# Kernel tuning notes

Measured on AMD Instinct MI355X. Metric: run time of the kernel, lower is better.

## Reference

```python
import jax, jax.numpy as jnp
import numpy as np

B, S, E, H = 4, 1024, 2048, 16
D = E // H  # head_dim = 128


def setup_inputs() -> dict:
    key = jax.random.key(0)
    k1, k2, k3, k4, k5 = jax.random.split(key, 5)
    scale = 1.0 / np.sqrt(E)
    return {
        "query": jax.random.normal(k1, (B, S, E), dtype=jnp.float32),
        "in_proj_weight": jax.random.normal(k2, (3 * E, E), dtype=jnp.float32) * scale,
        "in_proj_bias": jax.random.normal(k3, (3 * E,), dtype=jnp.float32) * 0.02,
        "out_proj_weight": jax.random.normal(k4, (E, E), dtype=jnp.float32) * scale,
        "out_proj_bias": jax.random.normal(k5, (E,), dtype=jnp.float32) * 0.02,
    }


def reference(query, in_proj_weight, in_proj_bias, out_proj_weight, out_proj_bias):
    b, s, e = query.shape
    d = e // H
    # fused QKV projection: [B,S,3E]
    proj = jnp.einsum("bse,fe->bsf", query, in_proj_weight) + in_proj_bias
    q, k, v = jnp.split(proj, 3, axis=-1)
    # [B,S,E] -> [B,H,S,D]
    def to_heads(t):
        return t.reshape(b, s, H, d).transpose(0, 2, 1, 3)
    q, k, v = to_heads(q), to_heads(k), to_heads(v)
    # scaled dot-product attention (non-causal, no mask, no dropout)
    scores = jnp.einsum("bhqd,bhkd->bhqk", q, k) / jnp.sqrt(jnp.asarray(d, q.dtype))
    attn = jax.nn.softmax(scores, axis=-1)
    ctx = jnp.einsum("bhqk,bhkd->bhqd", attn, v)
    # [B,H,S,D] -> [B,S,E]
    ctx = ctx.transpose(0, 2, 1, 3).reshape(b, s, e)
    out = jnp.einsum("bse,fe->bsf", ctx, out_proj_weight) + out_proj_bias
    return out
```

## Files before the change

kernel.cpp:

```cpp
#include <hip/hip_runtime.h>
#include <hip/hip_fp16.h>

#define F16 _Float16
typedef F16 f16x8 __attribute__((ext_vector_type(8)));
typedef F16 f16x4 __attribute__((ext_vector_type(4)));
typedef float f32x4 __attribute__((ext_vector_type(4)));

__global__ void cvt_f32_f16(const float* __restrict__ src, F16* __restrict__ dst, int n) {
    int idx = blockIdx.x * blockDim.x + threadIdx.x;
    int stride = gridDim.x * blockDim.x;
    for (int i = idx * 4; i < n; i += stride * 4) {
        float4 v = *reinterpret_cast<const float4*>(src + i);
        f16x4 o;
        o[0] = (F16)v.x; o[1] = (F16)v.y; o[2] = (F16)v.z; o[3] = (F16)v.w;
        *reinterpret_cast<f16x4*>(dst + i) = o;
    }
}

__device__ __forceinline__ void gl_lds16(const F16* g, F16* l) {
    __builtin_amdgcn_global_load_lds(
        (const __attribute__((address_space(1))) void*)g,
        (__attribute__((address_space(3))) void*)l, 16, 0, 0);
}

template <int EPI>
__global__ __launch_bounds__(512, 2) void gemm8(
    const F16* __restrict__ A, const F16* __restrict__ Bw, const float* __restrict__ bias,
    F16* __restrict__ q_ws, F16* __restrict__ k_ws, F16* __restrict__ v_ws,
    float* __restrict__ fout, int M, int N, int K)
{
    __shared__ __align__(16) F16 lds[2][4][8192];
    const int tid = threadIdx.x;
    const int w = tid >> 6, l = tid & 63;
    const int lr = l & 15, lg = l >> 4;
    const int wm = w >> 2, wn = w & 3;

    const int nbn = N >> 8;
    const int cpx = (int)gridDim.x >> 3;
    const int work = ((int)blockIdx.x & 7) * cpx + ((int)blockIdx.x >> 3);
    const int nb = work % nbn, mb = work / nbn;
    const long brow = (long)mb * 256, bcol = (long)nb * 256;

    const F16* rb0 = A + brow * K;
    const F16* rb1 = rb0 + 128 * (long)K;
    const F16* rb2 = Bw + bcol * K;
    const F16* rb3 = rb2 + 128 * (long)K;

    const int sr0 = ((tid >> 7) << 4) + (tid & 15);
    const int skk = (((tid >> 6) & 1) << 5) + (((tid >> 4) & 3) << 3);
    const int wb8 = (w << 6) * 8;

#define GISSUE(BUF, R, S, KT, RB) \
    gl_lds16(RB + (long)(sr0 + S * 64) * K + (KT) * 64 + skk, \
             &lds[BUF][R][S * 4096 + wb8])

    const int NK = K >> 6;

    f32x4 acc[8][4];
#pragma unroll
    for (int f = 0; f < 8; ++f)
#pragma unroll
        for (int nf = 0; nf < 4; ++nf) acc[f][nf] = f32x4{0.f, 0.f, 0.f, 0.f};

    GISSUE(0, 0, 0, 0, rb0); GISSUE(0, 0, 1, 0, rb0);
    GISSUE(0, 1, 0, 0, rb1); GISSUE(0, 1, 1, 0, rb1);
    GISSUE(0, 2, 0, 0, rb2); GISSUE(0, 2, 1, 0, rb2);
    GISSUE(0, 3, 0, 0, rb3); GISSUE(0, 3, 1, 0, rb3);
    if (NK > 1) {
        GISSUE(1, 2, 0, 1, rb2); GISSUE(1, 2, 1, 1, rb2);
        GISSUE(1, 3, 0, 1, rb3); GISSUE(1, 3, 1, 1, rb3);
        GISSUE(1, 0, 0, 1, rb0); GISSUE(1, 1, 0, 1, rb1);
        asm volatile("s_waitcnt vmcnt(6)" ::: "memory");
    } else {
        asm volatile("s_waitcnt vmcnt(0)" ::: "memory");
    }
    __builtin_amdgcn_s_barrier();

    for (int kt = 0; kt < NK; ++kt) {
        const int cur = kt & 1, nxt = cur ^ 1;
        const F16* Areg = &lds[cur][wm][0];
        const F16* Breg = &lds[cur][2 + (wn >> 1)][0];
        f16x8 b[4][2];
#pragma unroll
        for (int nf = 0; nf < 4; ++nf)
#pragma unroll
            for (int ks = 0; ks < 2; ++ks)
                b[nf][ks] = *reinterpret_cast<const f16x8*>(
                    Breg + ((((wn & 1) * 4 + nf) * 2 + ks) * 64 + l) * 8);
#pragma unroll
        for (int p = 0; p < 4; ++p) {
            f16x8 a[2][2];
#pragma unroll
            for (int mf = 0; mf < 2; ++mf)
#pragma unroll
                for (int ks = 0; ks < 2; ++ks)
                    a[mf][ks] = *reinterpret_cast<const f16x8*>(
                        Areg + (((2 * p + mf) * 2 + ks) * 64 + l) * 8);
            if (p == 0) {
                if (kt + 1 < NK) { GISSUE(nxt, 0, 1, kt + 1, rb0); GISSUE(nxt, 1, 1, kt + 1, rb1); }
            } else if (p == 1) {
                if (kt + 2 < NK) { GISSUE(cur, 2, 0, kt + 2, rb2); GISSUE(cur, 2, 1, kt + 2, rb2); }
            } else if (p == 2) {
                if (kt + 2 < NK) { GISSUE(cur, 3, 0, kt + 2, rb3); GISSUE(cur, 3, 1, kt + 2, rb3); }
            } else {
                if (kt + 2 < NK) { GISSUE(cur, 0, 0, kt + 2, rb0); GISSUE(cur, 1, 0, kt + 2, rb1); }
            }
            __builtin_amdgcn_sched_barrier(0);
            __builtin_amdgcn_s_barrier();
            asm volatile("s_waitcnt lgkmcnt(0)" ::: "memory");
            __builtin_amdgcn_sched_barrier(0);
            __builtin_amdgcn_s_setprio(1);
#pragma unroll
            for (int mf = 0; mf < 2; ++mf)
#pragma unroll
                for (int nf = 0; nf < 4; ++nf)
#pragma unroll
                    for (int ks = 0; ks < 2; ++ks)
                        acc[2 * p + mf][nf] = __builtin_amdgcn_mfma_f32_16x16x32_f16(
                            a[mf][ks], b[nf][ks], acc[2 * p + mf][nf], 0, 0, 0);
            __builtin_amdgcn_s_setprio(0);
            __builtin_amdgcn_sched_barrier(0);
            if (p == 3) {
                if (kt + 2 < NK) asm volatile("s_waitcnt vmcnt(6)" ::: "memory");
                else             asm volatile("s_waitcnt vmcnt(0)" ::: "memory");
            }
            __builtin_amdgcn_s_barrier();
        }
    }
#undef GISSUE

    const int col0 = (int)bcol + wn * 64;
    const int row0 = (int)brow + wm * 128;
    if constexpr (EPI == 0) {
        const int part = (int)(bcol >> 11);
        const int bI = row0 >> 10;
        const int sb = row0 & 1023;
        const float scl = (part == 0) ? 0.08838834764831845f : 1.0f;
#pragma unroll
        for (int nf = 0; nf < 4; ++nf) {
            const int gcol = col0 + nf * 16 + lr;
            const float bv = bias[gcol];
            const int d = gcol & 127;
            const int hh = (gcol >> 7) & 15;
            if (part == 2) {
                F16* dst0 = v_ws + ((long)((bI * 16 + hh) * 128 + d)) * 1024;
#pragma unroll
                for (int f = 0; f < 8; ++f) {
                    f16x4 pv;
#pragma unroll
                    for (int r = 0; r < 4; ++r) pv[r] = (F16)(acc[f][nf][r] + bv);
                    *reinterpret_cast<f16x4*>(dst0 + sb + f * 16 + lg * 4) = pv;
                }
            } else {
                F16* dst0 = ((part == 0) ? q_ws : k_ws) + ((long)(bI * 16 + hh) * 1024) * 128 + d;
#pragma unroll
                for (int f = 0; f < 8; ++f)
#pragma unroll
                    for (int r = 0; r < 4; ++r)
                        dst0[(long)(sb + f * 16 + lg * 4 + r) * 128] =
                            (F16)((acc[f][nf][r] + bv) * scl);
            }
        }
    } else {
#pragma unroll
        for (int nf = 0; nf < 4; ++nf) {
            const int gcol = col0 + nf * 16 + lr;
            const float bv = bias[gcol];
#pragma unroll
            for (int f = 0; f < 8; ++f)
#pragma unroll
                for (int r = 0; r < 4; ++r)
                    fout[(long)(row0 + f * 16 + lg * 4 + r) * N + gcol] = acc[f][nf][r] + bv;
        }
    }
}

__global__ __launch_bounds__(256, 2) void attn_kernel(
    const F16* __restrict__ q_ws, const F16* __restrict__ k_ws,
    const F16* __restrict__ v_ws, F16* __restrict__ ctx)
{
    __shared__ __align__(16) F16 kt[2][64 * 128];
    __shared__ __align__(16) F16 vt[2][128 * 64];
    __shared__ __align__(16) F16 p_lds[4][2048];
    const int tid = threadIdx.x;
    const int w = tid >> 6, l = tid & 63;
    const int lr = l & 15, lg = l >> 4;
    const int work = (blockIdx.x & 7) * 64 + (blockIdx.x >> 3);
    const int bh = work >> 3, qt = work & 7;
    const int b = bh >> 4, h = bh & 15;
    const int q0 = qt * 128 + w * 32;

    const F16* kbh = k_ws + (long)bh * 1024 * 128;
    const F16* vbh = v_ws + (long)bh * 128 * 1024;

    f16x8 qf[2][4];
#pragma unroll
    for (int mi = 0; mi < 2; ++mi)
#pragma unroll
        for (int ks = 0; ks < 4; ++ks)
            qf[mi][ks] = *reinterpret_cast<const f16x8*>(
                q_ws + ((long)bh * 1024 + q0 + mi * 16 + lr) * 128 + ks * 32 + lg * 8);

    auto stage = [&](int buf, int kv0) {
#pragma unroll
        for (int t = 0; t < 4; ++t) {
            const int chunk = t * 256 + tid;
            const int row = chunk >> 4;
            const int colb = (chunk & 15) << 4;
            const int gcol = colb ^ ((row & 7) << 4);
            gl_lds16(kbh + (long)(kv0 + row) * 128 + (gcol >> 1),
                     &kt[buf][(t * 256 + w * 64) * 8]);
        }
#pragma unroll
        for (int t = 0; t < 4; ++t) {
            const int chunk = t * 256 + tid;
            const int d = chunk >> 3;
            const int colb = (chunk & 7) << 4;
            const int gcol = colb ^ ((d & 7) << 4);
            gl_lds16(vbh + (long)d * 1024 + kv0 + (gcol >> 1),
                     &vt[buf][(t * 256 + w * 64) * 8]);
        }
    };

    float mrun[2][4], lsum[2][4];
#pragma unroll
    for (int mi = 0; mi < 2; ++mi)
#pragma unroll
        for (int r = 0; r < 4; ++r) { mrun[mi][r] = -1e30f; lsum[mi][r] = 0.f; }
    f32x4 acc[2][8];
#pragma unroll
    for (int mi = 0; mi < 2; ++mi)
#pragma unroll
        for (int nf = 0; nf < 8; ++nf) acc[mi][nf] = f32x4{0.f, 0.f, 0.f, 0.f};

    stage(0, 0);
    __syncthreads();
    int cur = 0;
    for (int it = 0; it < 16; ++it) {
        if (it + 1 < 16) stage(cur ^ 1, (it + 1) * 64);

        f32x4 sc[2][4];
#pragma unroll
        for (int mi = 0; mi < 2; ++mi)
#pragma unroll
            for (int cf = 0; cf < 4; ++cf) sc[mi][cf] = f32x4{0.f, 0.f, 0.f, 0.f};
#pragma unroll
        for (int cf = 0; cf < 4; ++cf) {
#pragma unroll
            for (int ks = 0; ks < 4; ++ks) {
                const int row = cf * 16 + lr;
                const int eff = (ks * 64 + lg * 16) ^ ((row & 7) << 4);
                f16x8 kf = *reinterpret_cast<const f16x8*>(&kt[cur][row * 128 + (eff >> 1)]);
#pragma unroll
                for (int mi = 0; mi < 2; ++mi)
                    sc[mi][cf] = __builtin_amdgcn_mfma_f32_16x16x32_f16(qf[mi][ks], kf, sc[mi][cf], 0, 0, 0);
            }
        }

#pragma unroll
        for (int mi = 0; mi < 2; ++mi) {
            float t4[4];
#pragma unroll
            for (int r = 0; r < 4; ++r)
                t4[r] = fmaxf(fmaxf(sc[mi][0][r], sc[mi][1][r]), fmaxf(sc[mi][2][r], sc[mi][3][r]));
#pragma unroll
            for (int msk = 1; msk < 16; msk <<= 1)
#pragma unroll
                for (int r = 0; r < 4; ++r) t4[r] = fmaxf(t4[r], __shfl_xor(t4[r], msk));
            float al[4], rs[4], p[4][4];
#pragma unroll
            for (int r = 0; r < 4; ++r) {
                const float mn = fmaxf(mrun[mi][r], t4[r]);
                al[r] = __expf(mrun[mi][r] - mn);
                mrun[mi][r] = mn;
#pragma unroll
                for (int cf = 0; cf < 4; ++cf) p[cf][r] = __expf(sc[mi][cf][r] - mn);
                rs[r] = (p[0][r] + p[1][r]) + (p[2][r] + p[3][r]);
            }
#pragma unroll
            for (int msk = 1; msk < 16; msk <<= 1)
#pragma unroll
                for (int r = 0; r < 4; ++r) rs[r] += __shfl_xor(rs[r], msk);
#pragma unroll
            for (int r = 0; r < 4; ++r) lsum[mi][r] = lsum[mi][r] * al[r] + rs[r];
#pragma unroll
            for (int nf = 0; nf < 8; ++nf)
#pragma unroll
                for (int r = 0; r < 4; ++r) acc[mi][nf][r] *= al[r];
#pragma unroll
            for (int cf = 0; cf < 4; ++cf)
#pragma unroll
                for (int r = 0; r < 4; ++r) {
                    const int chunk = (mi * 2 + (cf >> 1)) * 64 + (lg * 4 + r) + ((cf & 1) * 2 + (lr >> 3)) * 16;
                    p_lds[w][chunk * 8 + (lr & 7)] = (F16)p[cf][r];
                }
        }

        f16x8 pf[2][2];
#pragma unroll
        for (int mi = 0; mi < 2; ++mi)
#pragma unroll
            for (int half = 0; half < 2; ++half)
                pf[mi][half] = *reinterpret_cast<const f16x8*>(&p_lds[w][((mi * 2 + half) * 64 + l) * 8]);
#pragma unroll
        for (int nf = 0; nf < 8; ++nf) {
#pragma unroll
            for (int half = 0; half < 2; ++half) {
                const int d = nf * 16 + lr;
                const int eff = (half * 64 + lg * 16) ^ ((d & 7) << 4);
                f16x8 vf = *reinterpret_cast<const f16x8*>(&vt[cur][d * 64 + (eff >> 1)]);
#pragma unroll
                for (int mi = 0; mi < 2; ++mi)
                    acc[mi][nf] = __builtin_amdgcn_mfma_f32_16x16x32_f16(pf[mi][half], vf, acc[mi][nf], 0, 0, 0);
            }
        }
        __syncthreads();
        cur ^= 1;
    }

#pragma unroll
    for (int mi = 0; mi < 2; ++mi) {
        float inv[4];
#pragma unroll
        for (int r = 0; r < 4; ++r) inv[r] = 1.f / lsum[mi][r];
#pragma unroll
        for (int nf = 0; nf < 8; ++nf)
#pragma unroll
            for (int r = 0; r < 4; ++r) {
                const int s = q0 + mi * 16 + lg * 4 + r;
                const int e = h * 128 + nf * 16 + lr;
                ctx[((long)(b * 1024 + s)) * 2048 + e] = (F16)(acc[mi][nf][r] * inv[r]);
            }
    }
}

extern "C" void kernel_launch(void* const* d_in, const int* in_sizes, int n_in,
                              void* d_out, int out_size, void* d_ws, size_t ws_size,
                              hipStream_t stream) {
    const float* query = (const float*)d_in[0];
    const float* w_in  = (const float*)d_in[1];
    const float* b_in  = (const float*)d_in[2];
    const float* w_out = (const float*)d_in[3];
    const float* b_out = (const float*)d_in[4];
    float* out = (float*)d_out;

    char* ws = (char*)d_ws;
    size_t off = 0;
    auto carve = [&](size_t bytes) -> void* {
        void* p = ws + off;
        off += (bytes + 255) & ~(size_t)255;
        return p;
    };
    F16* xq  = (F16*)carve(8388608ULL * 2);
    F16* wih = (F16*)carve(12582912ULL * 2);
    F16* woh = (F16*)carve(4194304ULL * 2);
    F16* qws = (F16*)carve(8388608ULL * 2);
    F16* kws = (F16*)carve(8388608ULL * 2);
    F16* vws = (F16*)carve(8388608ULL * 2);
    F16* ctx = (F16*)carve(8388608ULL * 2);

    cvt_f32_f16<<<1024, 256, 0, stream>>>(query, xq, 8388608);
    cvt_f32_f16<<<1024, 256, 0, stream>>>(w_in, wih, 12582912);
    cvt_f32_f16<<<512, 256, 0, stream>>>(w_out, woh, 4194304);

    gemm8<0><<<384, 512, 0, stream>>>(xq, wih, b_in, qws, kws, vws, nullptr, 4096, 6144, 2048);
    attn_kernel<<<512, 256, 0, stream>>>(qws, kws, vws, ctx);
    gemm8<1><<<128, 512, 0, stream>>>(ctx, woh, b_out, nullptr, nullptr, nullptr, out, 4096, 2048, 2048);
}
```

Measured before the change: 418.5 us.

## Use 128x256 tiles for out-projection GEMM and remap block-to-XCD tiling

Splits the templated GEMM into a QKV kernel and a separate out-projection kernel. The out-projection now uses 128x256 tiles, launching 256 blocks instead of 128, to fill more of the 256 CUs, with a retuned double-buffered load pipeline and a smaller accumulator. Both kernels get an explicit block-to-XCD mapping so blocks on the same XCD share A and B panels in L2. The cost is lower per-block data reuse in the out-projection and a new pipeline schedule that has not been tuned yet.

```diff
diff --git a/kernel.cpp b/kernel.cpp
--- a/kernel.cpp
+++ b/kernel.cpp
@@ -23,11 +23,10 @@
         (__attribute__((address_space(3))) void*)l, 16, 0, 0);
 }
 
-template <int EPI>
-__global__ __launch_bounds__(512, 2) void gemm8(
+__global__ __launch_bounds__(512, 2) void gemm8qkv(
     const F16* __restrict__ A, const F16* __restrict__ Bw, const float* __restrict__ bias,
     F16* __restrict__ q_ws, F16* __restrict__ k_ws, F16* __restrict__ v_ws,
-    float* __restrict__ fout, int M, int N, int K)
+    int M, int N, int K)
 {
     __shared__ __align__(16) F16 lds[2][4][8192];
     const int tid = threadIdx.x;
@@ -35,10 +34,9 @@
     const int lr = l & 15, lg = l >> 4;
     const int wm = w >> 2, wn = w & 3;
 
-    const int nbn = N >> 8;
-    const int cpx = (int)gridDim.x >> 3;
-    const int work = ((int)blockIdx.x & 7) * cpx + ((int)blockIdx.x >> 3);
-    const int nb = work % nbn, mb = work / nbn;
+    const int xcd = (int)blockIdx.x & 7, s5 = (int)blockIdx.x >> 3;
+    const int mb = (xcd & 1) * 8 + s5 / 6;
+    const int nb = (xcd >> 1) * 6 + s5 % 6;
     const long brow = (long)mb * 256, bcol = (long)nb * 256;
 
     const F16* rb0 = A + brow * K;
@@ -131,47 +129,147 @@
 
     const int col0 = (int)bcol + wn * 64;
     const int row0 = (int)brow + wm * 128;
-    if constexpr (EPI == 0) {
-        const int part = (int)(bcol >> 11);
-        const int bI = row0 >> 10;
-        const int sb = row0 & 1023;
-        const float scl = (part == 0) ? 0.08838834764831845f : 1.0f;
-#pragma unroll
-        for (int nf = 0; nf < 4; ++nf) {
-            const int gcol = col0 + nf * 16 + lr;
-            const float bv = bias[gcol];
-            const int d = gcol & 127;
-            const int hh = (gcol >> 7) & 15;
-            if (part == 2) {
-                F16* dst0 = v_ws + ((long)((bI * 16 + hh) * 128 + d)) * 1024;
-#pragma unroll
-                for (int f = 0; f < 8; ++f) {
-                    f16x4 pv;
-#pragma unroll
-                    for (int r = 0; r < 4; ++r) pv[r] = (F16)(acc[f][nf][r] + bv);
-                    *reinterpret_cast<f16x4*>(dst0 + sb + f * 16 + lg * 4) = pv;
+    const int part = (int)(bcol >> 11);
+    const int bI = row0 >> 10;
+    const int sb = row0 & 1023;
+    const float scl = (part == 0) ? 0.08838834764831845f : 1.0f;
+#pragma unroll
+    for (int nf = 0; nf < 4; ++nf) {
+        const int gcol = col0 + nf * 16 + lr;
+        const float bv = bias[gcol];
+        const int d = gcol & 127;
+        const int hh = (gcol >> 7) & 15;
+        if (part == 2) {
+            F16* dst0 = v_ws + ((long)((bI * 16 + hh) * 128 + d)) * 1024;
+#pragma unroll
+            for (int f = 0; f < 8; ++f) {
+                f16x4 pv;
+#pragma unroll
+                for (int r = 0; r < 4; ++r) pv[r] = (F16)(acc[f][nf][r] + bv);
+                *reinterpret_cast<f16x4*>(dst0 + sb + f * 16 + lg * 4) = pv;
+            }
+        } else {
+            F16* dst0 = ((part == 0) ? q_ws : k_ws) + ((long)(bI * 16 + hh) * 1024) * 128 + d;
+#pragma unroll
+            for (int f = 0; f < 8; ++f)
+#pragma unroll
+                for (int r = 0; r < 4; ++r)
+                    dst0[(long)(sb + f * 16 + lg * 4 + r) * 128] =
+                        (F16)((acc[f][nf][r] + bv) * scl);
+        }
+    }
+}
+
+__global__ __launch_bounds__(512, 2) void gemm8out(
+    const F16* __restrict__ A, const F16* __restrict__ Bw, const float* __restrict__ bias,
+    float* __restrict__ fout, int M, int N, int K)
+{
+    __shared__ __align__(16) F16 lds[2][3][8192];
+    const int tid = threadIdx.x;
+    const int w = tid >> 6, l = tid & 63;
+    const int lr = l & 15, lg = l >> 4;
+    const int wm = w >> 2, wn = w & 3;
+
+    const int xcd = (int)blockIdx.x & 7, s5 = (int)blockIdx.x >> 3;
+    const int mb = (xcd & 3) * 8 + (s5 >> 2);
+    const int nb = (xcd >> 2) * 4 + (s5 & 3);
+    const long brow = (long)mb * 128, bcol = (long)nb * 256;
+
+    const F16* rbA = A + brow * K;
+    const F16* rb2 = Bw + bcol * K;
+    const F16* rb3 = rb2 + 128 * (long)K;
+
+    const int sr0 = ((tid >> 7) << 4) + (tid & 15);
+    const int skk = (((tid >> 6) & 1) << 5) + (((tid >> 4) & 3) << 3);
+    const int wb8 = (w << 6) * 8;
+
+#define GISSUE(BUF, R, S, KT, RB) \
+    gl_lds16(RB + (long)(sr0 + S * 64) * K + (KT) * 64 + skk, \
+             &lds[BUF][R][S * 4096 + wb8])
+
+    const int NK = K >> 6;
+
+    f32x4 acc[4][4];
+#pragma unroll
+    for (int f = 0; f < 4; ++f)
+#pragma unroll
+        for (int nf = 0; nf < 4; ++nf) acc[f][nf] = f32x4{0.f, 0.f, 0.f, 0.f};
+
+    GISSUE(0, 0, 0, 0, rbA); GISSUE(0, 0, 1, 0, rbA);
+    GISSUE(0, 1, 0, 0, rb2); GISSUE(0, 1, 1, 0, rb2);
+    GISSUE(0, 2, 0, 0, rb3); GISSUE(0, 2, 1, 0, rb3);
+    if (NK > 1) {
+        GISSUE(1, 1, 0, 1, rb2); GISSUE(1, 1, 1, 1, rb2);
+        GISSUE(1, 2, 0, 1, rb3); GISSUE(1, 2, 1, 1, rb3);
+        asm volatile("s_waitcnt vmcnt(4)" ::: "memory");
+    } else {
+        asm volatile("s_waitcnt vmcnt(0)" ::: "memory");
+    }
+    __builtin_amdgcn_s_barrier();
+
+    for (int kt = 0; kt < NK; ++kt) {
+        const int cur = kt & 1, nxt = cur ^ 1;
+        const F16* Areg = &lds[cur][0][0];
+        const F16* Breg = &lds[cur][1 + (wn >> 1)][0];
+        f16x8 b[4][2];
+#pragma unroll
+        for (int nf = 0; nf < 4; ++nf)
+#pragma unroll
+            for (int ks = 0; ks < 2; ++ks)
+                b[nf][ks] = *reinterpret_cast<const f16x8*>(
+                    Breg + ((((wn & 1) * 4 + nf) * 2 + ks) * 64 + l) * 8);
+#pragma unroll
+        for (int p = 0; p < 2; ++p) {
+            f16x8 a[2][2];
+#pragma unroll
+            for (int mf = 0; mf < 2; ++mf)
+#pragma unroll
+                for (int ks = 0; ks < 2; ++ks)
+                    a[mf][ks] = *reinterpret_cast<const f16x8*>(
+                        Areg + (((wm * 4 + 2 * p + mf) * 2 + ks) * 64 + l) * 8);
+            if (p == 0) {
+                if (kt + 1 < NK) { GISSUE(nxt, 0, 0, kt + 1, rbA); GISSUE(nxt, 0, 1, kt + 1, rbA); }
+            } else {
+                if (kt + 2 < NK) {
+                    GISSUE(cur, 1, 0, kt + 2, rb2); GISSUE(cur, 1, 1, kt + 2, rb2);
+                    GISSUE(cur, 2, 0, kt + 2, rb3); GISSUE(cur, 2, 1, kt + 2, rb3);
                 }
-            } else {
-                F16* dst0 = ((part == 0) ? q_ws : k_ws) + ((long)(bI * 16 + hh) * 1024) * 128 + d;
-#pragma unroll
-                for (int f = 0; f < 8; ++f)
-#pragma unroll
-                    for (int r = 0; r < 4; ++r)
-                        dst0[(long)(sb + f * 16 + lg * 4 + r) * 128] =
-                            (F16)((acc[f][nf][r] + bv) * scl);
-            }
-        }
-    } else {
-#pragma unroll
-        for (int nf = 0; nf < 4; ++nf) {
-            const int gcol = col0 + nf * 16 + lr;
-            const float bv = bias[gcol];
-#pragma unroll
-            for (int f = 0; f < 8; ++f)
-#pragma unroll
-                for (int r = 0; r < 4; ++r)
-                    fout[(long)(row0 + f * 16 + lg * 4 + r) * N + gcol] = acc[f][nf][r] + bv;
-        }
+            }
+            __builtin_amdgcn_sched_barrier(0);
+            __builtin_amdgcn_s_barrier();
+            asm volatile("s_waitcnt lgkmcnt(0)" ::: "memory");
+            __builtin_amdgcn_sched_barrier(0);
+            __builtin_amdgcn_s_setprio(1);
+#pragma unroll
+            for (int mf = 0; mf < 2; ++mf)
+#pragma unroll
+                for (int nf = 0; nf < 4; ++nf)
+#pragma unroll
+                    for (int ks = 0; ks < 2; ++ks)
+                        acc[2 * p + mf][nf] = __builtin_amdgcn_mfma_f32_16x16x32_f16(
+                            a[mf][ks], b[nf][ks], acc[2 * p + mf][nf], 0, 0, 0);
+            __builtin_amdgcn_s_setprio(0);
+            __builtin_amdgcn_sched_barrier(0);
+            if (p == 1) {
+                if (kt + 2 < NK) asm volatile("s_waitcnt vmcnt(4)" ::: "memory");
+                else             asm volatile("s_waitcnt vmcnt(0)" ::: "memory");
+            }
+            __builtin_amdgcn_s_barrier();
+        }
+    }
+#undef GISSUE
+
+    const int col0 = (int)bcol + wn * 64;
+    const int row0 = (int)brow + wm * 64;
+#pragma unroll
+    for (int nf = 0; nf < 4; ++nf) {
+        const int gcol = col0 + nf * 16 + lr;
+        const float bv = bias[gcol];
+#pragma unroll
+        for (int f = 0; f < 4; ++f)
+#pragma unroll
+            for (int r = 0; r < 4; ++r)
+                fout[(long)(row0 + f * 16 + lg * 4 + r) * N + gcol] = acc[f][nf][r] + bv;
     }
 }
 
@@ -363,7 +461,7 @@
     cvt_f32_f16<<<1024, 256, 0, stream>>>(w_in, wih, 12582912);
     cvt_f32_f16<<<512, 256, 0, stream>>>(w_out, woh, 4194304);
 
-    gemm8<0><<<384, 512, 0, stream>>>(xq, wih, b_in, qws, kws, vws, nullptr, 4096, 6144, 2048);
+    gemm8qkv<<<384, 512, 0, stream>>>(xq, wih, b_in, qws, kws, vws, 4096, 6144, 2048);
     attn_kernel<<<512, 256, 0, stream>>>(qws, kws, vws, ctx);
-    gemm8<1><<<128, 512, 0, stream>>>(ctx, woh, b_out, nullptr, nullptr, nullptr, out, 4096, 2048, 2048);
-}
+    gemm8out<<<256, 512, 0, stream>>>(ctx, woh, b_out, out, 4096, 2048, 2048);
+}
```

After: 402.8 us. 3.8% less time.
